# Kernel optimization log

Measured on AMD Instinct MI355X. Metric: run time of the kernel, lower is better.

Reference implementation:

```python
import jax, jax.numpy as jnp
import numpy as np

B, C, H = 4, 512, 4096
IC = C // 2


def setup_inputs() -> dict:
    key = jax.random.key(0)
    ks = jax.random.split(key, 9)
    s = 0.02
    return {
        "x": jax.random.normal(ks[0], (B, C, H), dtype=jnp.float32),
        "w_phi": jax.random.normal(ks[1], (IC, C), dtype=jnp.float32) * s,
        "b_phi": jax.random.normal(ks[2], (IC,), dtype=jnp.float32) * s,
        "w_theta": jax.random.normal(ks[3], (IC, C), dtype=jnp.float32) * s,
        "b_theta": jax.random.normal(ks[4], (IC,), dtype=jnp.float32) * s,
        "w_g": jax.random.normal(ks[5], (IC, C), dtype=jnp.float32) * s,
        "b_g": jax.random.normal(ks[6], (IC,), dtype=jnp.float32) * s,
        "w_mask": jax.random.normal(ks[7], (C, IC), dtype=jnp.float32) * s,
        "b_mask": jax.random.normal(ks[8], (C,), dtype=jnp.float32) * s,
    }


def reference(x, w_phi, b_phi, w_theta, b_theta, w_g, b_g, w_mask, b_mask):
    # conv1d kernel_size=1 == channel matmul. x: [b, c, h]
    phi = jnp.einsum('ic,bch->bih', w_phi, x) + b_phi[None, :, None]      # [b, ic, h]
    theta = jnp.einsum('ic,bch->bhi', w_theta, x) + b_theta[None, None, :]  # [b, h, ic]
    g = jnp.einsum('ic,bch->bhi', w_g, x) + b_g[None, None, :]             # [b, h, ic]
    scores = jnp.einsum('bqi,bik->bqk', theta, phi)                        # [b, h, h]
    # torch Softmax(dim=1) on [b, h_q, h_k] normalizes over the QUERY axis (axis=1)
    attn = jax.nn.softmax(scores, axis=1)
    ag = jnp.einsum('bqk,bki->bqi', attn, g)                               # [b, h, ic]
    mask = jnp.einsum('ci,bhi->bch', w_mask, ag) + b_mask[None, :, None]   # [b, c, h]
    return mask + x
```

## Files before the change

kernel.cpp:

```cpp
#include <hip/hip_runtime.h>
#include <hip/hip_bf16.h>
#include <hip/hip_fp16.h>
#include <type_traits>

constexpr int BB = 4;
constexpr int CC = 512;
constexpr int HH = 4096;
constexpr int IC = 256;

typedef _Float16 f16x8v __attribute__((ext_vector_type(8)));
typedef __bf16   bf16x8v __attribute__((ext_vector_type(8)));
typedef float    f32x4v __attribute__((ext_vector_type(4)));

__device__ __forceinline__ void gll16(const void* g, void* l) {
  __builtin_amdgcn_global_load_lds(
      (const __attribute__((address_space(1))) unsigned int*)g,
      (__attribute__((address_space(3))) unsigned int*)l, 16, 0, 0);
}

__device__ __forceinline__ f32x4v mfma16(f16x8v a, f16x8v b, f32x4v c) {
  return __builtin_amdgcn_mfma_f32_16x16x32_f16(a, b, c, 0, 0, 0);
}
__device__ __forceinline__ f32x4v mfma16(bf16x8v a, bf16x8v b, f32x4v c) {
  return __builtin_amdgcn_mfma_f32_16x16x32_bf16(a, b, c, 0, 0, 0);
}

__device__ __forceinline__ unsigned short hbits(float f) {
  __half h = __float2half(f);
  unsigned short b; __builtin_memcpy(&b, &h, 2); return b;
}
__device__ __forceinline__ unsigned short bbits(float f) {
  __hip_bfloat16 h = __float2bfloat16(f);
  unsigned short b; __builtin_memcpy(&b, &h, 2); return b;
}

template <int MODE>
__launch_bounds__(256)
__global__ void mgemm128(const void* __restrict__ Aall, const void* __restrict__ Ball,
                         const void* __restrict__ Ball2,
                         void* __restrict__ outP, void* __restrict__ out2P,
                         const float* __restrict__ bias, const float* __restrict__ bias2,
                         const float* __restrict__ xres, float* __restrict__ Z,
                         int M, int N, int K,
                         size_t sAb, size_t sBb, size_t sOb) {
  using ET = typename std::conditional<MODE == 3, bf16x8v, f16x8v>::type;

  __shared__ __align__(16) unsigned short sA[128 * 32];
  __shared__ __align__(16) unsigned short sB[128 * 32];

  const int zz = blockIdx.z;
  int b, which;
  if constexpr (MODE == 0) { b = zz & (BB - 1); which = zz >> 2; }
  else { b = zz; which = 0; }

  const unsigned short* __restrict__ A = (const unsigned short*)Aall + (size_t)b * sAb;
  const unsigned short* __restrict__ Bm =
      (const unsigned short*)((MODE == 0 && which) ? Ball2 : Ball) + (size_t)b * sBb;
  const float* __restrict__ biasSel = (MODE == 0 && which) ? bias2 : bias;
  void* __restrict__ outSel = (MODE == 0 && which) ? out2P : outP;

  const int t = threadIdx.x;
  const int lane = t & 63;
  const int w = t >> 6;
  const int wm = (w >> 1) << 6;
  const int wn = (w & 1) << 6;
  const int mBase = blockIdx.y * 128;
  const int nBase = blockIdx.x * 128;

  const int fr = lane & 15;
  const int fo = (lane >> 4) << 3;

  f32x4v acc[4][4] = {};

  for (int k0 = 0; k0 < K; k0 += 32) {
#pragma unroll
    for (int p = 0; p < 2; ++p) {
      const int u = t + (p << 8);
      const int r = u >> 2;
      const int cs = (u & 3) << 3;
      gll16(A + (size_t)(mBase + r) * K + (k0 + cs), sA + u * 8);
      gll16(Bm + (size_t)(nBase + r) * K + (k0 + cs), sB + u * 8);
    }
    __syncthreads();
    ET af[4], bf[4];
#pragma unroll
    for (int i = 0; i < 4; ++i)
      af[i] = *(const ET*)(sA + ((wm + (i << 4) + fr) << 5) + fo);
#pragma unroll
    for (int j = 0; j < 4; ++j)
      bf[j] = *(const ET*)(sB + ((wn + (j << 4) + fr) << 5) + fo);
#pragma unroll
    for (int i = 0; i < 4; ++i)
#pragma unroll
      for (int j = 0; j < 4; ++j)
        acc[i][j] = mfma16(af[i], bf[j], acc[i][j]);
    __syncthreads();
  }

  const int row0 = (lane >> 4) << 2;
  const int col = lane & 15;

  if constexpr (MODE == 2) {
    __hip_bfloat16* __restrict__ outB = (__hip_bfloat16*)outP;
    float csum[4] = {0.f, 0.f, 0.f, 0.f};
#pragma unroll
    for (int i = 0; i < 4; ++i) {
      const int m0 = mBase + wm + (i << 4) + row0;
#pragma unroll
      for (int j = 0; j < 4; ++j) {
        const int n = nBase + wn + (j << 4) + col;
        __hip_bfloat16* dst = outB + (size_t)b * sOb + (size_t)m0 * N + n;
#pragma unroll
        for (int rg = 0; rg < 4; ++rg) {
          const float e = __expf(acc[i][j][rg]);
          dst[(size_t)rg * N] = __float2bfloat16(e);
          csum[j] += e;
        }
      }
    }
#pragma unroll
    for (int j = 0; j < 4; ++j) {
      float s = csum[j];
      s += __shfl_xor(s, 16, 64);
      s += __shfl_xor(s, 32, 64);
      if (lane < 16) {
        const int n = nBase + wn + (j << 4) + col;
        atomicAdd(&Z[(size_t)b * N + n], s);
      }
    }
  } else {
#pragma unroll
    for (int i = 0; i < 4; ++i) {
      const int m0 = mBase + wm + (i << 4) + row0;
#pragma unroll
      for (int j = 0; j < 4; ++j) {
        const int n = nBase + wn + (j << 4) + col;
#pragma unroll
        for (int rg = 0; rg < 4; ++rg) {
          const int m = m0 + rg;
          const float v = acc[i][j][rg];
          if constexpr (MODE == 0) {
            ((__half*)outSel)[(size_t)b * sOb + (size_t)m * N + n] =
                __float2half(v + biasSel[n]);
          } else if constexpr (MODE == 1) {
            ((__hip_bfloat16*)outP)[(size_t)b * sOb + (size_t)m * N + n] =
                __float2bfloat16(v + bias[m]);
          } else {
            const size_t o = (size_t)b * sOb + (size_t)m * N + n;
            ((float*)outP)[o] = v + bias[m] + xres[o];
          }
        }
      }
    }
  }
}

__launch_bounds__(256)
__global__ void mgemm_ag(const __hip_bfloat16* __restrict__ Gall,
                         const __hip_bfloat16* __restrict__ Eall,
                         unsigned short* __restrict__ P16) {
  constexpr int KC = 1024;
  __shared__ __align__(16) unsigned short sA[256 * 32];
  __shared__ __align__(16) unsigned short sB[64 * 32];

  const int b = blockIdx.z;
  const int kc = blockIdx.x;
  const int qBase = blockIdx.y * 64;
  const int k0base = kc * KC;

  const unsigned short* __restrict__ G =
      (const unsigned short*)Gall + (size_t)b * IC * HH;
  const unsigned short* __restrict__ E =
      (const unsigned short*)Eall + (size_t)b * HH * HH;

  const int t = threadIdx.x;
  const int lane = t & 63;
  const int w = t >> 6;
  const int fr = lane & 15;
  const int fo = (lane >> 4) << 3;

  f32x4v acc[4][4] = {};

  for (int kk = 0; kk < KC; kk += 32) {
    const int k0 = k0base + kk;
#pragma unroll
    for (int p = 0; p < 4; ++p) {
      const int u = t + (p << 8);
      const int r = u >> 2;
      const int cs = (u & 3) << 3;
      gll16(G + (size_t)r * HH + (k0 + cs), sA + u * 8);
    }
    {
      const int r = t >> 2;
      const int cs = (t & 3) << 3;
      gll16(E + (size_t)(qBase + r) * HH + (k0 + cs), sB + t * 8);
    }
    __syncthreads();
    bf16x8v af[4], bf[4];
#pragma unroll
    for (int i = 0; i < 4; ++i)
      af[i] = *(const bf16x8v*)(sA + (((w << 6) + (i << 4) + fr) << 5) + fo);
#pragma unroll
    for (int j = 0; j < 4; ++j)
      bf[j] = *(const bf16x8v*)(sB + (((j << 4) + fr) << 5) + fo);
#pragma unroll
    for (int i = 0; i < 4; ++i)
#pragma unroll
      for (int j = 0; j < 4; ++j)
        acc[i][j] = mfma16(af[i], bf[j], acc[i][j]);
    __syncthreads();
  }

  unsigned short* __restrict__ P =
      P16 + ((size_t)kc * BB + b) * HH * IC;
  const int quad = lane >> 4;
  const int col = lane & 15;
#pragma unroll
  for (int i = 0; i < 4; ++i) {
    const int ic0 = (w << 6) + (i << 4) + (quad << 2);
#pragma unroll
    for (int j = 0; j < 4; ++j) {
      const int q = qBase + (j << 4) + col;
      ushort4 s = {hbits(acc[i][j][0]), hbits(acc[i][j][1]),
                   hbits(acc[i][j][2]), hbits(acc[i][j][3])};
      *(ushort4*)(P + (size_t)q * IC + ic0) = s;
    }
  }
}

__launch_bounds__(256)
__global__ void cvt_ag(const unsigned short* __restrict__ P16,
                       __hip_bfloat16* __restrict__ agB) {
  constexpr size_t CH = (size_t)BB * HH * IC;
  const size_t tIdx = (size_t)blockIdx.x * 256 + threadIdx.x;
  const f16x8v v0 = ((const f16x8v*)(P16))[tIdx];
  const f16x8v v1 = ((const f16x8v*)(P16 + CH))[tIdx];
  const f16x8v v2 = ((const f16x8v*)(P16 + 2 * CH))[tIdx];
  const f16x8v v3 = ((const f16x8v*)(P16 + 3 * CH))[tIdx];
  unsigned short o[8];
#pragma unroll
  for (int k = 0; k < 8; ++k) {
    const float s = (float)v0[k] + (float)v1[k] + (float)v2[k] + (float)v3[k];
    o[k] = bbits(s);
  }
  uint4 pack;
  __builtin_memcpy(&pack, o, 16);
  ((uint4*)agB)[tIdx] = pack;
}

__launch_bounds__(256)
__global__ void xpose(const float* __restrict__ x, __half* __restrict__ xT) {
  __shared__ float tile[64][65];
  const int b = blockIdx.z;
  const int h0 = blockIdx.x * 64;
  const int c0 = blockIdx.y * 64;
  const int lane = threadIdx.x & 63;
  const int r0 = threadIdx.x >> 6;
  const float* xb = x + (size_t)b * CC * HH;
#pragma unroll
  for (int rr = 0; rr < 16; ++rr) {
    const int c = r0 * 16 + rr;
    tile[c][lane] = xb[(size_t)(c0 + c) * HH + h0 + lane];
  }
  __syncthreads();
  __half* ob = xT + (size_t)b * HH * CC;
#pragma unroll
  for (int rr = 0; rr < 16; ++rr) {
    const int hl = r0 * 16 + rr;
    ob[(size_t)(h0 + hl) * CC + c0 + lane] = __float2half(tile[lane][hl]);
  }
}

__global__ void convw(const float* __restrict__ s0, const float* __restrict__ s1,
                      const float* __restrict__ s2, const float* __restrict__ s3,
                      __half* __restrict__ d0, __half* __restrict__ d1,
                      __half* __restrict__ d2, __hip_bfloat16* __restrict__ d3) {
  const int which = blockIdx.y;
  const int i = (blockIdx.x * 256 + threadIdx.x) * 4;
  if (which < 3) {
    const float* s = which == 0 ? s0 : (which == 1 ? s1 : s2);
    __half* d = which == 0 ? d0 : (which == 1 ? d1 : d2);
    const float4 v = *(const float4*)(s + i);
    d[i] = __float2half(v.x); d[i + 1] = __float2half(v.y);
    d[i + 2] = __float2half(v.z); d[i + 3] = __float2half(v.w);
  } else {
    const float4 v = *(const float4*)(s3 + i);
    d3[i] = __float2bfloat16(v.x); d3[i + 1] = __float2bfloat16(v.y);
    d3[i + 2] = __float2bfloat16(v.z); d3[i + 3] = __float2bfloat16(v.w);
  }
}

__launch_bounds__(256)
__global__ void gscale(unsigned int* __restrict__ g, const float* __restrict__ Z) {
  const size_t tid = (size_t)blockIdx.x * 256 + threadIdx.x;
  const size_t e0 = tid * 8;
  const int b = (int)(e0 >> 20);
  const int h = (int)(e0 & (HH - 1));
  const float* Zp = Z + ((size_t)b << 12) + h;
  uint4 raw = ((const uint4*)g)[tid];
  unsigned short* u = (unsigned short*)&raw;
#pragma unroll
  for (int k = 0; k < 8; ++k) {
    const float f = __uint_as_float(((unsigned)u[k]) << 16) / Zp[k];
    u[k] = bbits(f);
  }
  ((uint4*)g)[tid] = raw;
}

extern "C" void kernel_launch(void* const* d_in, const int* in_sizes, int n_in,
                              void* d_out, int out_size, void* d_ws, size_t ws_size,
                              hipStream_t stream) {
  (void)in_sizes; (void)n_in; (void)out_size; (void)ws_size;

  const float* x       = (const float*)d_in[0];
  const float* w_phi   = (const float*)d_in[1];
  const float* b_phi   = (const float*)d_in[2];
  const float* w_theta = (const float*)d_in[3];
  const float* b_theta = (const float*)d_in[4];
  const float* w_g     = (const float*)d_in[5];
  const float* b_g     = (const float*)d_in[6];
  const float* w_mask  = (const float*)d_in[7];
  const float* b_mask  = (const float*)d_in[8];
  float* out = (float*)d_out;

  char* p = (char*)d_ws;
  __hip_bfloat16* E = (__hip_bfloat16*)p;           p += (size_t)BB * HH * HH * 2;
  __half* xT       = (__half*)p;                    p += (size_t)BB * HH * CC * 2;
  __half* thetaH   = (__half*)p;                    p += (size_t)BB * HH * IC * 2;
  __half* phiH     = (__half*)p;                    p += (size_t)BB * HH * IC * 2;
  __hip_bfloat16* gB  = (__hip_bfloat16*)p;         p += (size_t)BB * IC * HH * 2;
  __hip_bfloat16* agB = (__hip_bfloat16*)p;         p += (size_t)BB * HH * IC * 2;
  __half* wthH = (__half*)p;                        p += (size_t)IC * CC * 2;
  __half* wphH = (__half*)p;                        p += (size_t)IC * CC * 2;
  __half* wgH  = (__half*)p;                        p += (size_t)IC * CC * 2;
  __hip_bfloat16* wmB = (__hip_bfloat16*)p;         p += (size_t)CC * IC * 2;
  float* Z = (float*)p;                             p += (size_t)BB * HH * 4;
  unsigned short* P16 = (unsigned short*)xT;

  const dim3 blk(256);

  convw<<<dim3(128, 4), blk, 0, stream>>>(w_phi, w_theta, w_g, w_mask, wphH, wthH, wgH, wmB);
  xpose<<<dim3(HH / 64, CC / 64, BB), blk, 0, stream>>>(x, xT);

  mgemm128<0><<<dim3(IC / 128, HH / 128, BB * 2), blk, 0, stream>>>(
      xT, wthH, wphH, thetaH, phiH, b_theta, b_phi, nullptr, nullptr,
      HH, IC, CC, (size_t)HH * CC, 0, (size_t)HH * IC);

  mgemm128<1><<<dim3(HH / 128, IC / 128, BB), blk, 0, stream>>>(
      wgH, xT, nullptr, gB, nullptr, b_g, nullptr, nullptr, nullptr,
      IC, HH, CC, 0, (size_t)HH * CC, (size_t)IC * HH);

  hipMemsetAsync(Z, 0, (size_t)BB * HH * sizeof(float), stream);
  mgemm128<2><<<dim3(HH / 128, HH / 128, BB), blk, 0, stream>>>(
      thetaH, phiH, nullptr, E, nullptr, nullptr, nullptr, nullptr, Z,
      HH, HH, IC, (size_t)HH * IC, (size_t)HH * IC, (size_t)HH * HH);

  gscale<<<dim3((BB * IC * HH / 8) / 256), blk, 0, stream>>>((unsigned int*)gB, Z);

  mgemm_ag<<<dim3(4, HH / 64, BB), blk, 0, stream>>>(gB, E, P16);
  cvt_ag<<<dim3((BB * HH * IC / 8) / 256), blk, 0, stream>>>(P16, agB);

  mgemm128<3><<<dim3(HH / 128, CC / 128, BB), blk, 0, stream>>>(
      wmB, agB, nullptr, out, nullptr, b_mask, nullptr, x, nullptr,
      CC, HH, IC, 0, (size_t)HH * IC, (size_t)CC * HH);
}
```

Measured before the change: 291.6 us.

## Double-buffer LDS tiles in GEMMs and swap operands for vectorized transposed stores

Adds double-buffered shared-memory staging to both GEMM kernels so the global-to-LDS loads for the next K-slice are issued while MFMAs run on the current one, removing one barrier per iteration. It also swaps the A/B operands of every mgemm128 launch so each lane's four accumulator rows are contiguous in memory. That lets the epilogues write ushort4/float4 vectors instead of scalar strided stores, with the softmax column sums reduced by lane shuffles. LDS use doubles per block, which may lower occupancy.

```diff
diff --git a/kernel.cpp b/kernel.cpp
--- a/kernel.cpp
+++ b/kernel.cpp
@@ -36,28 +36,29 @@
 
 template <int MODE>
 __launch_bounds__(256)
-__global__ void mgemm128(const void* __restrict__ Aall, const void* __restrict__ Ball,
-                         const void* __restrict__ Ball2,
-                         void* __restrict__ outP, void* __restrict__ out2P,
-                         const float* __restrict__ bias, const float* __restrict__ bias2,
+__global__ void mgemm128(const void* __restrict__ A0, const void* __restrict__ A1,
+                         const void* __restrict__ B0,
+                         void* __restrict__ out0, void* __restrict__ out1,
+                         const float* __restrict__ bias0, const float* __restrict__ bias1,
                          const float* __restrict__ xres, float* __restrict__ Z,
                          int M, int N, int K,
                          size_t sAb, size_t sBb, size_t sOb) {
   using ET = typename std::conditional<MODE == 3, bf16x8v, f16x8v>::type;
 
-  __shared__ __align__(16) unsigned short sA[128 * 32];
-  __shared__ __align__(16) unsigned short sB[128 * 32];
+  __shared__ __align__(16) unsigned short sA[2][128 * 32];
+  __shared__ __align__(16) unsigned short sB[2][128 * 32];
 
   const int zz = blockIdx.z;
   int b, which;
   if constexpr (MODE == 0) { b = zz & (BB - 1); which = zz >> 2; }
   else { b = zz; which = 0; }
 
-  const unsigned short* __restrict__ A = (const unsigned short*)Aall + (size_t)b * sAb;
+  const unsigned short* __restrict__ A =
+      (const unsigned short*)((MODE == 0 && which) ? A1 : A0) + (size_t)b * sAb;
   const unsigned short* __restrict__ Bm =
-      (const unsigned short*)((MODE == 0 && which) ? Ball2 : Ball) + (size_t)b * sBb;
-  const float* __restrict__ biasSel = (MODE == 0 && which) ? bias2 : bias;
-  void* __restrict__ outSel = (MODE == 0 && which) ? out2P : outP;
+      (const unsigned short*)B0 + (size_t)b * sBb;
+  const float* __restrict__ biasSel = (MODE == 0 && which) ? bias1 : bias0;
+  void* __restrict__ outSel = (MODE == 0 && which) ? out1 : out0;
 
   const int t = threadIdx.x;
   const int lane = t & 63;
@@ -72,83 +73,110 @@
 
   f32x4v acc[4][4] = {};
 
-  for (int k0 = 0; k0 < K; k0 += 32) {
+  auto stage = [&](int bi, int k0) {
 #pragma unroll
     for (int p = 0; p < 2; ++p) {
       const int u = t + (p << 8);
       const int r = u >> 2;
       const int cs = (u & 3) << 3;
-      gll16(A + (size_t)(mBase + r) * K + (k0 + cs), sA + u * 8);
-      gll16(Bm + (size_t)(nBase + r) * K + (k0 + cs), sB + u * 8);
-    }
+      gll16(A + (size_t)(mBase + r) * K + (k0 + cs), sA[bi] + u * 8);
+      gll16(Bm + (size_t)(nBase + r) * K + (k0 + cs), sB[bi] + u * 8);
+    }
+  };
+
+  stage(0, 0);
+  __syncthreads();
+  int cur = 0;
+  for (int k0 = 0; k0 < K; k0 += 32) {
+    if (k0 + 32 < K) stage(cur ^ 1, k0 + 32);
+    ET af[4], bfv[4];
+#pragma unroll
+    for (int i = 0; i < 4; ++i)
+      af[i] = *(const ET*)(sA[cur] + ((wm + (i << 4) + fr) << 5) + fo);
+#pragma unroll
+    for (int j = 0; j < 4; ++j)
+      bfv[j] = *(const ET*)(sB[cur] + ((wn + (j << 4) + fr) << 5) + fo);
+#pragma unroll
+    for (int i = 0; i < 4; ++i)
+#pragma unroll
+      for (int j = 0; j < 4; ++j)
+        acc[i][j] = mfma16(af[i], bfv[j], acc[i][j]);
     __syncthreads();
-    ET af[4], bf[4];
-#pragma unroll
-    for (int i = 0; i < 4; ++i)
-      af[i] = *(const ET*)(sA + ((wm + (i << 4) + fr) << 5) + fo);
-#pragma unroll
-    for (int j = 0; j < 4; ++j)
-      bf[j] = *(const ET*)(sB + ((wn + (j << 4) + fr) << 5) + fo);
-#pragma unroll
-    for (int i = 0; i < 4; ++i)
-#pragma unroll
-      for (int j = 0; j < 4; ++j)
-        acc[i][j] = mfma16(af[i], bf[j], acc[i][j]);
-    __syncthreads();
-  }
-
-  const int row0 = (lane >> 4) << 2;
+    cur ^= 1;
+  }
+
+  const int quad = lane >> 4;
   const int col = lane & 15;
 
   if constexpr (MODE == 2) {
-    __hip_bfloat16* __restrict__ outB = (__hip_bfloat16*)outP;
-    float csum[4] = {0.f, 0.f, 0.f, 0.f};
+    unsigned short* __restrict__ outB = (unsigned short*)out0;
+    float zp[4][4];
+#pragma unroll
+    for (int i = 0; i < 4; ++i)
+#pragma unroll
+      for (int r = 0; r < 4; ++r) zp[i][r] = 0.f;
 #pragma unroll
     for (int i = 0; i < 4; ++i) {
-      const int m0 = mBase + wm + (i << 4) + row0;
+      const int kk0 = mBase + wm + (i << 4) + (quad << 2);
+#pragma unroll
+      for (int j = 0; j < 4; ++j) {
+        const int q = nBase + wn + (j << 4) + col;
+        const float e0 = __expf(acc[i][j][0]);
+        const float e1 = __expf(acc[i][j][1]);
+        const float e2 = __expf(acc[i][j][2]);
+        const float e3 = __expf(acc[i][j][3]);
+        zp[i][0] += e0; zp[i][1] += e1; zp[i][2] += e2; zp[i][3] += e3;
+        ushort4 s = {bbits(e0), bbits(e1), bbits(e2), bbits(e3)};
+        *(ushort4*)(outB + (size_t)b * sOb + (size_t)q * M + kk0) = s;
+      }
+    }
+#pragma unroll
+    for (int i = 0; i < 4; ++i)
+#pragma unroll
+      for (int r = 0; r < 4; ++r) {
+        float s = zp[i][r];
+        s += __shfl_xor(s, 1, 64);
+        s += __shfl_xor(s, 2, 64);
+        s += __shfl_xor(s, 4, 64);
+        s += __shfl_xor(s, 8, 64);
+        zp[i][r] = s;
+      }
+    if (col == 0) {
+#pragma unroll
+      for (int i = 0; i < 4; ++i) {
+        const int kk0 = mBase + wm + (i << 4) + (quad << 2);
+#pragma unroll
+        for (int r = 0; r < 4; ++r)
+          atomicAdd(&Z[(size_t)b * M + kk0 + r], zp[i][r]);
+      }
+    }
+  } else {
+#pragma unroll
+    for (int i = 0; i < 4; ++i) {
+      const int m0 = mBase + wm + (i << 4) + (quad << 2);
+      float4 bv;
+      if constexpr (MODE == 0) bv = *(const float4*)(biasSel + m0);
 #pragma unroll
       for (int j = 0; j < 4; ++j) {
         const int n = nBase + wn + (j << 4) + col;
-        __hip_bfloat16* dst = outB + (size_t)b * sOb + (size_t)m0 * N + n;
-#pragma unroll
-        for (int rg = 0; rg < 4; ++rg) {
-          const float e = __expf(acc[i][j][rg]);
-          dst[(size_t)rg * N] = __float2bfloat16(e);
-          csum[j] += e;
-        }
-      }
-    }
-#pragma unroll
-    for (int j = 0; j < 4; ++j) {
-      float s = csum[j];
-      s += __shfl_xor(s, 16, 64);
-      s += __shfl_xor(s, 32, 64);
-      if (lane < 16) {
-        const int n = nBase + wn + (j << 4) + col;
-        atomicAdd(&Z[(size_t)b * N + n], s);
-      }
-    }
-  } else {
-#pragma unroll
-    for (int i = 0; i < 4; ++i) {
-      const int m0 = mBase + wm + (i << 4) + row0;
-#pragma unroll
-      for (int j = 0; j < 4; ++j) {
-        const int n = nBase + wn + (j << 4) + col;
-#pragma unroll
-        for (int rg = 0; rg < 4; ++rg) {
-          const int m = m0 + rg;
-          const float v = acc[i][j][rg];
-          if constexpr (MODE == 0) {
-            ((__half*)outSel)[(size_t)b * sOb + (size_t)m * N + n] =
-                __float2half(v + biasSel[n]);
-          } else if constexpr (MODE == 1) {
-            ((__hip_bfloat16*)outP)[(size_t)b * sOb + (size_t)m * N + n] =
-                __float2bfloat16(v + bias[m]);
-          } else {
-            const size_t o = (size_t)b * sOb + (size_t)m * N + n;
-            ((float*)outP)[o] = v + bias[m] + xres[o];
-          }
+        if constexpr (MODE == 0) {
+          ushort4 s = {hbits(acc[i][j][0] + bv.x), hbits(acc[i][j][1] + bv.y),
+                       hbits(acc[i][j][2] + bv.z), hbits(acc[i][j][3] + bv.w)};
+          *(ushort4*)((unsigned short*)outSel + (size_t)b * sOb +
+                      (size_t)n * M + m0) = s;
+        } else if constexpr (MODE == 1) {
+          const float bn = bias0[n];
+          ushort4 s = {bbits(acc[i][j][0] + bn), bbits(acc[i][j][1] + bn),
+                       bbits(acc[i][j][2] + bn), bbits(acc[i][j][3] + bn)};
+          *(ushort4*)((unsigned short*)out0 + (size_t)b * sOb +
+                      (size_t)n * M + m0) = s;
+        } else {
+          const float bn = bias0[n];
+          const size_t o = (size_t)b * sOb + (size_t)n * M + m0;
+          const float4 xv = *(const float4*)(xres + o);
+          float4 ov = {acc[i][j][0] + bn + xv.x, acc[i][j][1] + bn + xv.y,
+                       acc[i][j][2] + bn + xv.z, acc[i][j][3] + bn + xv.w};
+          *(float4*)((float*)out0 + o) = ov;
         }
       }
     }
@@ -160,8 +188,8 @@
                          const __hip_bfloat16* __restrict__ Eall,
                          unsigned short* __restrict__ P16) {
   constexpr int KC = 1024;
-  __shared__ __align__(16) unsigned short sA[256 * 32];
-  __shared__ __align__(16) unsigned short sB[64 * 32];
+  __shared__ __align__(16) unsigned short sA[2][256 * 32];
+  __shared__ __align__(16) unsigned short sB[2][64 * 32];
 
   const int b = blockIdx.z;
   const int kc = blockIdx.x;
@@ -181,34 +209,40 @@
 
   f32x4v acc[4][4] = {};
 
-  for (int kk = 0; kk < KC; kk += 32) {
-    const int k0 = k0base + kk;
+  auto stage = [&](int bi, int k0) {
 #pragma unroll
     for (int p = 0; p < 4; ++p) {
       const int u = t + (p << 8);
       const int r = u >> 2;
       const int cs = (u & 3) << 3;
-      gll16(G + (size_t)r * HH + (k0 + cs), sA + u * 8);
+      gll16(G + (size_t)r * HH + (k0 + cs), sA[bi] + u * 8);
     }
     {
       const int r = t >> 2;
       const int cs = (t & 3) << 3;
-      gll16(E + (size_t)(qBase + r) * HH + (k0 + cs), sB + t * 8);
-    }
+      gll16(E + (size_t)(qBase + r) * HH + (k0 + cs), sB[bi] + t * 8);
+    }
+  };
+
+  stage(0, k0base);
+  __syncthreads();
+  int cur = 0;
+  for (int kk = 0; kk < KC; kk += 32) {
+    if (kk + 32 < KC) stage(cur ^ 1, k0base + kk + 32);
+    bf16x8v af[4], bfv[4];
+#pragma unroll
+    for (int i = 0; i < 4; ++i)
+      af[i] = *(const bf16x8v*)(sA[cur] + (((w << 6) + (i << 4) + fr) << 5) + fo);
+#pragma unroll
+    for (int j = 0; j < 4; ++j)
+      bfv[j] = *(const bf16x8v*)(sB[cur] + (((j << 4) + fr) << 5) + fo);
+#pragma unroll
+    for (int i = 0; i < 4; ++i)
+#pragma unroll
+      for (int j = 0; j < 4; ++j)
+        acc[i][j] = mfma16(af[i], bfv[j], acc[i][j]);
     __syncthreads();
-    bf16x8v af[4], bf[4];
-#pragma unroll
-    for (int i = 0; i < 4; ++i)
-      af[i] = *(const bf16x8v*)(sA + (((w << 6) + (i << 4) + fr) << 5) + fo);
-#pragma unroll
-    for (int j = 0; j < 4; ++j)
-      bf[j] = *(const bf16x8v*)(sB + (((j << 4) + fr) << 5) + fo);
-#pragma unroll
-    for (int i = 0; i < 4; ++i)
-#pragma unroll
-      for (int j = 0; j < 4; ++j)
-        acc[i][j] = mfma16(af[i], bf[j], acc[i][j]);
-    __syncthreads();
+    cur ^= 1;
   }
 
   unsigned short* __restrict__ P =
@@ -342,17 +376,17 @@
   convw<<<dim3(128, 4), blk, 0, stream>>>(w_phi, w_theta, w_g, w_mask, wphH, wthH, wgH, wmB);
   xpose<<<dim3(HH / 64, CC / 64, BB), blk, 0, stream>>>(x, xT);
 
-  mgemm128<0><<<dim3(IC / 128, HH / 128, BB * 2), blk, 0, stream>>>(
-      xT, wthH, wphH, thetaH, phiH, b_theta, b_phi, nullptr, nullptr,
-      HH, IC, CC, (size_t)HH * CC, 0, (size_t)HH * IC);
-
-  mgemm128<1><<<dim3(HH / 128, IC / 128, BB), blk, 0, stream>>>(
-      wgH, xT, nullptr, gB, nullptr, b_g, nullptr, nullptr, nullptr,
-      IC, HH, CC, 0, (size_t)HH * CC, (size_t)IC * HH);
+  mgemm128<0><<<dim3(HH / 128, IC / 128, BB * 2), blk, 0, stream>>>(
+      wthH, wphH, xT, thetaH, phiH, b_theta, b_phi, nullptr, nullptr,
+      IC, HH, CC, 0, (size_t)HH * CC, (size_t)HH * IC);
+
+  mgemm128<1><<<dim3(IC / 128, HH / 128, BB), blk, 0, stream>>>(
+      xT, nullptr, wgH, gB, nullptr, b_g, nullptr, nullptr, nullptr,
+      HH, IC, CC, (size_t)HH * CC, 0, (size_t)IC * HH);
 
   hipMemsetAsync(Z, 0, (size_t)BB * HH * sizeof(float), stream);
   mgemm128<2><<<dim3(HH / 128, HH / 128, BB), blk, 0, stream>>>(
-      thetaH, phiH, nullptr, E, nullptr, nullptr, nullptr, nullptr, Z,
+      phiH, nullptr, thetaH, E, nullptr, nullptr, nullptr, nullptr, Z,
       HH, HH, IC, (size_t)HH * IC, (size_t)HH * IC, (size_t)HH * HH);
 
   gscale<<<dim3((BB * IC * HH / 8) / 256), blk, 0, stream>>>((unsigned int*)gB, Z);
@@ -360,7 +394,7 @@
   mgemm_ag<<<dim3(4, HH / 64, BB), blk, 0, stream>>>(gB, E, P16);
   cvt_ag<<<dim3((BB * HH * IC / 8) / 256), blk, 0, stream>>>(P16, agB);
 
-  mgemm128<3><<<dim3(HH / 128, CC / 128, BB), blk, 0, stream>>>(
-      wmB, agB, nullptr, out, nullptr, b_mask, nullptr, x, nullptr,
-      CC, HH, IC, 0, (size_t)HH * IC, (size_t)CC * HH);
-}
+  mgemm128<3><<<dim3(CC / 128, HH / 128, BB), blk, 0, stream>>>(
+      agB, nullptr, wmB, out, nullptr, b_mask, nullptr, x, nullptr,
+      HH, CC, IC, (size_t)HH * IC, 0, (size_t)CC * HH);
+}
```

After: 327.3 us. +12.2%, slower.

## Widen attn·g k-tile to 128 with XOR-swizzled LDS and halve split-K

Applied to the files above, without the earlier changes.

The attn·g GEMM now stages 128-wide k tiles of G and E in LDS with an XOR swizzle on 16-byte chunks, so fragment reads avoid bank conflicts and each barrier covers four MFMA k-steps instead of one. The split-K factor drops from 4 to 2, so fewer fp16 partial buffers are written and the conversion kernel sums two partials instead of four. The trade-offs are a grid half as large, which may lower occupancy and wave count, and roughly 80KB of LDS per block, which limits how many blocks fit on a CU.

```diff
diff --git a/kernel.cpp b/kernel.cpp
--- a/kernel.cpp
+++ b/kernel.cpp
@@ -159,9 +159,10 @@
 __global__ void mgemm_ag(const __hip_bfloat16* __restrict__ Gall,
                          const __hip_bfloat16* __restrict__ Eall,
                          unsigned short* __restrict__ P16) {
-  constexpr int KC = 1024;
-  __shared__ __align__(16) unsigned short sA[256 * 32];
-  __shared__ __align__(16) unsigned short sB[64 * 32];
+  constexpr int KC = 2048;
+  constexpr int BK = 128;
+  __shared__ __align__(16) unsigned short sG[256 * BK];
+  __shared__ __align__(16) unsigned short sE[64 * BK];
 
   const int b = blockIdx.z;
   const int kc = blockIdx.x;
@@ -178,36 +179,47 @@
   const int w = t >> 6;
   const int fr = lane & 15;
   const int fo = (lane >> 4) << 3;
+  const int fc = fo >> 3;
 
   f32x4v acc[4][4] = {};
 
-  for (int kk = 0; kk < KC; kk += 32) {
+  for (int kk = 0; kk < KC; kk += BK) {
     const int k0 = k0base + kk;
 #pragma unroll
     for (int p = 0; p < 4; ++p) {
       const int u = t + (p << 8);
-      const int r = u >> 2;
-      const int cs = (u & 3) << 3;
-      gll16(G + (size_t)r * HH + (k0 + cs), sA + u * 8);
-    }
-    {
-      const int r = t >> 2;
-      const int cs = (t & 3) << 3;
-      gll16(E + (size_t)(qBase + r) * HH + (k0 + cs), sB + t * 8);
+      const int row = u >> 4;
+      const int csrc = (u & 15) ^ (row & 7);
+      gll16(E + (size_t)(qBase + row) * HH + k0 + (csrc << 3), sE + u * 8);
+    }
+#pragma unroll
+    for (int p = 0; p < 16; ++p) {
+      const int u = t + (p << 8);
+      const int row = u >> 4;
+      const int csrc = (u & 15) ^ (row & 7);
+      gll16(G + (size_t)row * HH + k0 + (csrc << 3), sG + u * 8);
     }
     __syncthreads();
-    bf16x8v af[4], bf[4];
-#pragma unroll
-    for (int i = 0; i < 4; ++i)
-      af[i] = *(const bf16x8v*)(sA + (((w << 6) + (i << 4) + fr) << 5) + fo);
-#pragma unroll
-    for (int j = 0; j < 4; ++j)
-      bf[j] = *(const bf16x8v*)(sB + (((j << 4) + fr) << 5) + fo);
-#pragma unroll
-    for (int i = 0; i < 4; ++i)
-#pragma unroll
-      for (int j = 0; j < 4; ++j)
-        acc[i][j] = mfma16(af[i], bf[j], acc[i][j]);
+#pragma unroll
+    for (int ks = 0; ks < 4; ++ks) {
+      bf16x8v af[4], bfv[4];
+      const int c16 = (ks << 2) + fc;
+#pragma unroll
+      for (int i = 0; i < 4; ++i) {
+        const int row = (w << 6) + (i << 4) + fr;
+        af[i] = *(const bf16x8v*)(sG + row * BK + ((c16 ^ (row & 7)) << 3));
+      }
+#pragma unroll
+      for (int j = 0; j < 4; ++j) {
+        const int row = (j << 4) + fr;
+        bfv[j] = *(const bf16x8v*)(sE + row * BK + ((c16 ^ (row & 7)) << 3));
+      }
+#pragma unroll
+      for (int i = 0; i < 4; ++i)
+#pragma unroll
+        for (int j = 0; j < 4; ++j)
+          acc[i][j] = mfma16(af[i], bfv[j], acc[i][j]);
+    }
     __syncthreads();
   }
 
@@ -235,12 +247,10 @@
   const size_t tIdx = (size_t)blockIdx.x * 256 + threadIdx.x;
   const f16x8v v0 = ((const f16x8v*)(P16))[tIdx];
   const f16x8v v1 = ((const f16x8v*)(P16 + CH))[tIdx];
-  const f16x8v v2 = ((const f16x8v*)(P16 + 2 * CH))[tIdx];
-  const f16x8v v3 = ((const f16x8v*)(P16 + 3 * CH))[tIdx];
   unsigned short o[8];
 #pragma unroll
   for (int k = 0; k < 8; ++k) {
-    const float s = (float)v0[k] + (float)v1[k] + (float)v2[k] + (float)v3[k];
+    const float s = (float)v0[k] + (float)v1[k];
     o[k] = bbits(s);
   }
   uint4 pack;
@@ -357,7 +367,7 @@
 
   gscale<<<dim3((BB * IC * HH / 8) / 256), blk, 0, stream>>>((unsigned int*)gB, Z);
 
-  mgemm_ag<<<dim3(4, HH / 64, BB), blk, 0, stream>>>(gB, E, P16);
+  mgemm_ag<<<dim3(2, HH / 64, BB), blk, 0, stream>>>(gB, E, P16);
   cvt_ag<<<dim3((BB * HH * IC / 8) / 256), blk, 0, stream>>>(P16, agB);
 
   mgemm128<3><<<dim3(HH / 128, CC / 128, BB), blk, 0, stream>>>(
```

New measurement: 266.9 us. 1.09x faster.
